# Kernel tuning notes

Hardware: AMD Instinct MI355X
Metric: run time of the kernel (lower is better)

The kernel has to match this reference:

```python
import jax, jax.numpy as jnp
import numpy as np

BATCH = 1024
D_IN = 4096
D_OUT = 4096
B = 128  # block size
K_IN = (D_IN + B - 1) // B    # 32
K_OUT = (D_OUT + B - 1) // B  # 32


def setup_inputs() -> dict:
    key = jax.random.key(0)
    kx, kw, kd = jax.random.split(key, 3)
    x = jax.random.normal(kx, (BATCH, D_IN), dtype=jnp.float32)
    W = jax.random.normal(kw, (K_OUT, K_IN, B), dtype=jnp.float32) * 0.1
    # Bernoulli +/-1 diagonal
    D_bernoulli = jnp.where(jax.random.bernoulli(kd, p=0.5, shape=(D_IN,)), 1.0, -1.0).astype(jnp.float32)
    return {"x": x, "W": W, "D_bernoulli": D_bernoulli}


def reference(x, W, D_bernoulli):
    k_out, k_in, b = W.shape
    d_in = D_IN
    d_out = D_OUT
    if x.ndim == 1:
        x = x[None, :]
    batch = x.shape[0]
    # diagonal sign flip
    x_d = x * D_bernoulli[None, :]
    pad_len = k_in * b - d_in
    if pad_len > 0:
        x_d = jnp.pad(x_d, ((0, 0), (0, pad_len)))
    x_blocks = x_d.reshape(batch, k_in, b)
    # frequency-domain block-circulant matmul
    X_fft = jnp.fft.fft(x_blocks, axis=-1)            # (batch, k_in, b) complex
    W_fft = jnp.fft.fft(W, axis=-1)                    # (k_out, k_in, b) complex
    # Y_fft[n,o,:] = sum_j X_fft[n,j,:] * conj(W_fft[o,j,:])
    Y_fft = jnp.einsum('njb,ojb->nob', X_fft, jnp.conjugate(W_fft))
    Y = jnp.fft.ifft(Y_fft, axis=-1).real              # (batch, k_out, b)
    out_flat = Y.reshape(batch, k_out * b)
    if k_out * b > d_out:
        out_flat = out_flat[:, :d_out]
    return out_flat
```

## Files before the change

kernel.cpp:

```cpp
#include <hip/hip_runtime.h>
#include <hip/hip_bf16.h>

#define TWOPI_OVER_B 0.049087385212340517f

typedef __attribute__((ext_vector_type(8))) short bf16x8;
typedef __attribute__((ext_vector_type(4))) float f32x4;

static __device__ __forceinline__ unsigned short f2bf(float f) {
    __hip_bfloat16 h = __float2bfloat16(f);
    return *reinterpret_cast<unsigned short*>(&h);
}
static __device__ __forceinline__ unsigned long long pack4(float a, float b, float c, float d) {
    return (unsigned long long)f2bf(a) | ((unsigned long long)f2bf(b) << 16)
         | ((unsigned long long)f2bf(c) << 32) | ((unsigned long long)f2bf(d) << 48);
}

__global__ __launch_bounds__(256) void k_prep(const float* __restrict__ W,
                                              unsigned short* __restrict__ fragB,
                                              unsigned short* __restrict__ fragCi,
                                              unsigned short* __restrict__ BmatT) {
    __shared__ char smem[73984];
    int tid = threadIdx.x;

    if (blockIdx.x < 80) {
        int i = blockIdx.x * 256 + tid;
        if (i < 18432) {
            int e = i & 7, l2 = (i >> 3) & 63, kb = (i >> 9) & 3, c = i >> 11;
            int kr = c * 16 + (l2 & 15);
            int t  = kb * 32 + (l2 >> 4) * 8 + e;
            float v = 0.f;
            if (kr < 65)       v =  cosf(TWOPI_OVER_B * (float)((kr * t) & 127));
            else if (kr < 130) v = -sinf(TWOPI_OVER_B * (float)(((kr - 65) * t) & 127));
            fragB[i] = f2bf(v);
        }
        if (i < 20480) {
            int e = i & 7, l2 = (i >> 3) & 63;
            int ckb = i >> 9; int kb = ckb % 5, c = ckb / 5;
            int kr = kb * 32 + (l2 >> 4) * 8 + e;
            int t  = c * 16 + (l2 & 15);
            float v = 0.f;
            if (kr < 65)       v =  cosf(TWOPI_OVER_B * (float)((kr * t) & 127));
            else if (kr < 130) v = -sinf(TWOPI_OVER_B * (float)(((kr - 65) * t) & 127));
            fragCi[i] = f2bf(v);
        }
        return;
    }

    int bw = blockIdx.x - 80;
    unsigned long long* xs8 = (unsigned long long*)smem;
    float* Yl = (float*)smem;
    unsigned short* fB = (unsigned short*)(smem + 37120);

    for (int i = tid; i < 18432; i += 256) {
        int e = i & 7, l2 = (i >> 3) & 63, kb = (i >> 9) & 3, c = i >> 11;
        int kr = c * 16 + (l2 & 15);
        int t  = kb * 32 + (l2 >> 4) * 8 + e;
        float v = 0.f;
        if (kr < 65)       v =  cosf(TWOPI_OVER_B * (float)((kr * t) & 127));
        else if (kr < 130) v = -sinf(TWOPI_OVER_B * (float)(((kr - 65) * t) & 127));
        fB[i] = f2bf(v);
    }
    #pragma unroll
    for (int it = 0; it < 8; ++it) {
        int f  = tid + it * 256;
        float4 wa = ((const float4*)W)[(size_t)bw * 2048 + f];
        int rl = f >> 5;
        int t0 = (f & 31) * 4;
        int byte = (rl * 256 + t0 * 2) ^ ((rl & 7) << 4);
        xs8[byte >> 3] = pack4(wa.x, wa.y, wa.z, wa.w);
    }
    __syncthreads();

    int l = tid & 63, w = tid >> 6;
    int rl_a = w * 16 + (l & 15);
    int coff = (l >> 4) * 16;
    bf16x8 a[4];
    #pragma unroll
    for (int kb = 0; kb < 4; ++kb) {
        int byte = (rl_a * 256 + kb * 64 + coff) ^ ((rl_a & 7) << 4);
        a[kb] = *(const bf16x8*)(smem + byte);
    }
    __syncthreads();

    f32x4 acc[9];
    #pragma unroll
    for (int c = 0; c < 9; ++c) acc[c] = (f32x4)0.f;
    #pragma unroll
    for (int c = 0; c < 9; ++c)
        #pragma unroll
        for (int kb = 0; kb < 4; ++kb)
            acc[c] = __builtin_amdgcn_mfma_f32_16x16x32_bf16(a[kb], ((const bf16x8*)fB)[(c * 4 + kb) * 64 + l], acc[c], 0, 0, 0);

    int rowd = w * 16 + (l >> 4) * 4;
    int cold = l & 15;
    #pragma unroll
    for (int c = 0; c < 9; ++c)
        #pragma unroll
        for (int r = 0; r < 4; ++r)
            Yl[(rowd + r) * 145 + c * 16 + cold] = acc[c][r];
    __syncthreads();

    int o0 = bw * 2;
    for (int c2 = tid; c2 < 4160; c2 += 256) {
        int k = c2 >> 6, sub = c2 & 63;
        int oo = sub >> 5, h = (sub >> 4) & 1, t = sub & 15;
        int j0 = t * 4;
        float sc = (k == 0 || k == 64) ? (1.f / 128.f) : (2.f / 128.f);
        int col; float sgn;
        if (j0 < 32) { col = h ? 65 + k : k;  sgn = h ? -sc : sc; }
        else         { col = h ? k : 65 + k;  sgn = sc; }
        int rlb = oo * 32 + (j0 & 31);
        unsigned long long pk = pack4(sgn * Yl[(rlb + 0) * 145 + col], sgn * Yl[(rlb + 1) * 145 + col],
                                      sgn * Yl[(rlb + 2) * 145 + col], sgn * Yl[(rlb + 3) * 145 + col]);
        int o2 = h * 32 + o0 + oo;
        *(unsigned long long*)(BmatT + ((size_t)k * 64 + o2) * 64 + j0) = pk;
    }
}

#define YS_OFF 33280
__global__ __launch_bounds__(512, 4) void k_fused(const float* __restrict__ x,
                                                  const float* __restrict__ D,
                                                  const bf16x8* __restrict__ fragB,
                                                  const bf16x8* __restrict__ fragCi,
                                                  const unsigned short* __restrict__ BmatT,
                                                  float* __restrict__ out) {
    __shared__ char smem[74240];
    unsigned long long* xs8 = (unsigned long long*)smem;
    int tid = threadIdx.x, l = tid & 63, w = tid >> 6;
    int lr = l & 15, lq = l >> 4;
    int n0 = blockIdx.x * 4;

    #pragma unroll
    for (int it = 0; it < 8; ++it) {
        int f  = tid + it * 512;
        int nn = f >> 10, f4 = f & 1023;
        float4 xa = ((const float4*)(x + (size_t)(n0 + nn) * 4096))[f4];
        float4 da = ((const float4*)D)[f4];
        int rl = nn * 32 + (f4 >> 5);
        int t0 = (f4 & 31) * 4;
        int byte = (rl * 256 + t0 * 2) ^ ((rl & 7) << 4);
        xs8[byte >> 3] = pack4(xa.x * da.x, xa.y * da.y, xa.z * da.z, xa.w * da.w);
    }
    for (int i = tid; i < 3840; i += 512) {
        int rl = i / 30, cp = 130 + i % 30;
        int byte = (rl * 320 + cp * 2) ^ ((rl & 7) << 4);
        *(unsigned short*)(smem + YS_OFF + byte) = 0;
    }
    __syncthreads();

    int rl_a = w * 16 + lr;
    bf16x8 a[4];
    #pragma unroll
    for (int kb = 0; kb < 4; ++kb) {
        int byte = (rl_a * 256 + kb * 64 + lq * 16) ^ ((rl_a & 7) << 4);
        a[kb] = *(const bf16x8*)(smem + byte);
    }
    __syncthreads();

    {
        f32x4 acc[9];
        #pragma unroll
        for (int c = 0; c < 9; ++c) acc[c] = (f32x4)0.f;
        #pragma unroll
        for (int c = 0; c < 9; ++c)
            #pragma unroll
            for (int kb = 0; kb < 4; ++kb)
                acc[c] = __builtin_amdgcn_mfma_f32_16x16x32_bf16(a[kb], fragB[(c * 4 + kb) * 64 + l], acc[c], 0, 0, 0);

        int rowbase = w * 16 + lq * 4;
        #pragma unroll
        for (int c = 0; c < 9; ++c) {
            int col = c * 16 + lr;
            if (col < 130) {
                int k, reim;
                if (col < 65) { k = col;      reim = 0; }
                else          { k = col - 65; reim = 32; }
                #pragma unroll
                for (int rr = 0; rr < 4; ++rr) {
                    int rl2 = rowbase + rr;
                    int nn = rl2 >> 5, j = rl2 & 31;
                    int byte = (k * 512 + nn * 128 + (reim + j) * 2) ^ ((k & 7) << 4);
                    *(unsigned short*)(smem + byte) = f2bf(acc[c][rr]);
                }
            }
        }
    }
    __syncthreads();

    for (int k = w; k < 65; k += 8) {
        int xb = k * 512;
        int swz = (k & 7) << 4;
        bf16x8 a2[2];
        a2[0] = *(const bf16x8*)(smem + ((xb + (lr & 3) * 128 +      lq * 16) ^ swz));
        a2[1] = *(const bf16x8*)(smem + ((xb + (lr & 3) * 128 + 64 + lq * 16) ^ swz));
        const unsigned short* bb = BmatT + (size_t)k * 4096 + lr * 64 + lq * 8;
        f32x4 acc2[4];
        #pragma unroll
        for (int cf = 0; cf < 4; ++cf) acc2[cf] = (f32x4)0.f;
        #pragma unroll
        for (int cf = 0; cf < 4; ++cf) {
            bf16x8 b0 = *(const bf16x8*)(bb + cf * 1024);
            bf16x8 b1 = *(const bf16x8*)(bb + cf * 1024 + 32);
            acc2[cf] = __builtin_amdgcn_mfma_f32_16x16x32_bf16(a2[0], b0, acc2[cf], 0, 0, 0);
            acc2[cf] = __builtin_amdgcn_mfma_f32_16x16x32_bf16(a2[1], b1, acc2[cf], 0, 0, 0);
        }
        if (lq == 0) {
            #pragma unroll
            for (int cf = 0; cf < 4; ++cf) {
                int o2  = cf * 16 + lr;
                int col = (o2 < 32) ? k : 65 + k;
                #pragma unroll
                for (int rr = 0; rr < 4; ++rr) {
                    int row2 = rr * 32 + (o2 & 31);
                    int byte = (row2 * 320 + col * 2) ^ ((row2 & 7) << 4);
                    *(unsigned short*)(smem + YS_OFF + byte) = f2bf(acc2[cf][rr]);
                }
            }
        }
    }
    __syncthreads();

    {
        bf16x8 ac[5];
        #pragma unroll
        for (int kb = 0; kb < 5; ++kb) {
            int byte = (rl_a * 320 + kb * 64 + lq * 16) ^ ((rl_a & 7) << 4);
            ac[kb] = *(const bf16x8*)(smem + YS_OFF + byte);
        }
        f32x4 acc3[8];
        #pragma unroll
        for (int c = 0; c < 8; ++c) acc3[c] = (f32x4)0.f;
        #pragma unroll
        for (int c = 0; c < 8; ++c)
            #pragma unroll
            for (int kb = 0; kb < 5; ++kb)
                acc3[c] = __builtin_amdgcn_mfma_f32_16x16x32_bf16(ac[kb], fragCi[(c * 5 + kb) * 64 + l], acc3[c], 0, 0, 0);

        int rowd = blockIdx.x * 128 + w * 16 + lq * 4;
        #pragma unroll
        for (int c = 0; c < 8; ++c)
            #pragma unroll
            for (int r = 0; r < 4; ++r)
                out[(size_t)(rowd + r) * 128 + c * 16 + lr] = acc3[c][r];
    }
}

extern "C" void kernel_launch(void* const* d_in, const int* in_sizes, int n_in,
                              void* d_out, int out_size, void* d_ws, size_t ws_size,
                              hipStream_t stream) {
    const float* x = (const float*)d_in[0];
    const float* W = (const float*)d_in[1];
    const float* D = (const float*)d_in[2];
    float* out = (float*)d_out;

    unsigned short* BmatT  = (unsigned short*)d_ws;
    unsigned short* fragB  = BmatT + 266240;
    unsigned short* fragCi = fragB + 18432;

    k_prep <<<96, 256, 0, stream>>>(W, fragB, fragCi, BmatT);
    k_fused<<<256, 512, 0, stream>>>(x, D, (const bf16x8*)fragB, (const bf16x8*)fragCi, BmatT, out);
}
```

Before: 50.33 us.

## Halve rows per fused block, prefetch DFT fragments, use sincos table in prep

Fused kernel now processes 2 batch rows per 256-thread block (512 blocks) instead of 4 rows per 512-thread block. Frequency-domain staging moves to a separate LDS region with packed 64-bit writes, which drops one barrier. Global loads of the DFT and weight fragments are software-prefetched one iteration ahead of the MFMAs. k_prep computes a shared cos/sin table once instead of calling transcendentals per element. Smaller blocks should improve occupancy and latency hiding, but each block reloads BmatT for half as many rows, which doubles total weight traffic.

```diff
diff --git a/kernel.cpp b/kernel.cpp
--- a/kernel.cpp
+++ b/kernel.cpp
@@ -20,6 +20,7 @@
                                               unsigned short* __restrict__ fragCi,
                                               unsigned short* __restrict__ BmatT) {
     __shared__ char smem[73984];
+    __shared__ float tbl[256];
     int tid = threadIdx.x;
 
     if (blockIdx.x < 80) {
@@ -51,13 +52,20 @@
     float* Yl = (float*)smem;
     unsigned short* fB = (unsigned short*)(smem + 37120);
 
+    for (int i = tid; i < 128; i += 256) {
+        float s, c;
+        sincosf(TWOPI_OVER_B * (float)i, &s, &c);
+        tbl[i] = c; tbl[128 + i] = s;
+    }
+    __syncthreads();
+
     for (int i = tid; i < 18432; i += 256) {
         int e = i & 7, l2 = (i >> 3) & 63, kb = (i >> 9) & 3, c = i >> 11;
         int kr = c * 16 + (l2 & 15);
         int t  = kb * 32 + (l2 >> 4) * 8 + e;
         float v = 0.f;
-        if (kr < 65)       v =  cosf(TWOPI_OVER_B * (float)((kr * t) & 127));
-        else if (kr < 130) v = -sinf(TWOPI_OVER_B * (float)(((kr - 65) * t) & 127));
+        if (kr < 65)       v =  tbl[(kr * t) & 127];
+        else if (kr < 130) v = -tbl[128 + (((kr - 65) * t) & 127)];
         fB[i] = f2bf(v);
     }
     #pragma unroll
@@ -117,22 +125,23 @@
     }
 }
 
-#define YS_OFF 33280
-__global__ __launch_bounds__(512, 4) void k_fused(const float* __restrict__ x,
-                                                  const float* __restrict__ D,
-                                                  const bf16x8* __restrict__ fragB,
-                                                  const bf16x8* __restrict__ fragCi,
-                                                  const unsigned short* __restrict__ BmatT,
-                                                  float* __restrict__ out) {
-    __shared__ char smem[74240];
+#define XL_OFF 16384
+#define YS_OFF 33024
+__global__ __launch_bounds__(256) void k_fused(const float* __restrict__ x,
+                                               const float* __restrict__ D,
+                                               const bf16x8* __restrict__ fragB,
+                                               const bf16x8* __restrict__ fragCi,
+                                               const unsigned short* __restrict__ BmatT,
+                                               float* __restrict__ out) {
+    __shared__ char smem[53504];
     unsigned long long* xs8 = (unsigned long long*)smem;
     int tid = threadIdx.x, l = tid & 63, w = tid >> 6;
     int lr = l & 15, lq = l >> 4;
-    int n0 = blockIdx.x * 4;
+    int n0 = blockIdx.x * 2;
 
     #pragma unroll
     for (int it = 0; it < 8; ++it) {
-        int f  = tid + it * 512;
+        int f  = tid + it * 256;
         int nn = f >> 10, f4 = f & 1023;
         float4 xa = ((const float4*)(x + (size_t)(n0 + nn) * 4096))[f4];
         float4 da = ((const float4*)D)[f4];
@@ -141,7 +150,7 @@
         int byte = (rl * 256 + t0 * 2) ^ ((rl & 7) << 4);
         xs8[byte >> 3] = pack4(xa.x * da.x, xa.y * da.y, xa.z * da.z, xa.w * da.w);
     }
-    for (int i = tid; i < 3840; i += 512) {
+    for (int i = tid; i < 1920; i += 256) {
         int rl = i / 30, cp = 130 + i % 30;
         int byte = (rl * 320 + cp * 2) ^ ((rl & 7) << 4);
         *(unsigned short*)(smem + YS_OFF + byte) = 0;
@@ -155,66 +164,90 @@
         int byte = (rl_a * 256 + kb * 64 + lq * 16) ^ ((rl_a & 7) << 4);
         a[kb] = *(const bf16x8*)(smem + byte);
     }
-    __syncthreads();
-
     {
+        bf16x8 fb[4], fbn[4];
+        #pragma unroll
+        for (int kb = 0; kb < 4; ++kb) fb[kb] = fragB[kb * 64 + l];
         f32x4 acc[9];
         #pragma unroll
         for (int c = 0; c < 9; ++c) acc[c] = (f32x4)0.f;
         #pragma unroll
-        for (int c = 0; c < 9; ++c)
+        for (int c = 0; c < 9; ++c) {
+            if (c < 8) {
+                #pragma unroll
+                for (int kb = 0; kb < 4; ++kb) fbn[kb] = fragB[((c + 1) * 4 + kb) * 64 + l];
+            }
             #pragma unroll
             for (int kb = 0; kb < 4; ++kb)
-                acc[c] = __builtin_amdgcn_mfma_f32_16x16x32_bf16(a[kb], fragB[(c * 4 + kb) * 64 + l], acc[c], 0, 0, 0);
-
+                acc[c] = __builtin_amdgcn_mfma_f32_16x16x32_bf16(a[kb], fb[kb], acc[c], 0, 0, 0);
+            #pragma unroll
+            for (int kb = 0; kb < 4; ++kb) fb[kb] = fbn[kb];
+        }
         int rowbase = w * 16 + lq * 4;
+        int nn = rowbase >> 5, j0 = rowbase & 31;
         #pragma unroll
         for (int c = 0; c < 9; ++c) {
             int col = c * 16 + lr;
             if (col < 130) {
-                int k, reim;
-                if (col < 65) { k = col;      reim = 0; }
-                else          { k = col - 65; reim = 32; }
+                int k   = (col < 65) ? col : col - 65;
+                int off = (col < 65) ? 0 : 64;
+                unsigned long long pk = pack4(acc[c][0], acc[c][1], acc[c][2], acc[c][3]);
+                int byte = (k * 256 + nn * 128 + off + j0 * 2) ^ ((k & 7) << 4);
+                *(unsigned long long*)(smem + XL_OFF + byte) = pk;
+            }
+        }
+    }
+    __syncthreads();
+
+    {
+        bf16x8 b[4][2], nb[4][2];
+        {
+            const unsigned short* bb = BmatT + (size_t)w * 4096 + lr * 64 + lq * 8;
+            #pragma unroll
+            for (int cf = 0; cf < 4; ++cf) {
+                b[cf][0] = *(const bf16x8*)(bb + cf * 1024);
+                b[cf][1] = *(const bf16x8*)(bb + cf * 1024 + 32);
+            }
+        }
+        for (int k = w; k < 65; k += 4) {
+            int kn = k + 4;
+            if (kn < 65) {
+                const unsigned short* bb = BmatT + (size_t)kn * 4096 + lr * 64 + lq * 8;
                 #pragma unroll
-                for (int rr = 0; rr < 4; ++rr) {
-                    int rl2 = rowbase + rr;
-                    int nn = rl2 >> 5, j = rl2 & 31;
-                    int byte = (k * 512 + nn * 128 + (reim + j) * 2) ^ ((k & 7) << 4);
-                    *(unsigned short*)(smem + byte) = f2bf(acc[c][rr]);
+                for (int cf = 0; cf < 4; ++cf) {
+                    nb[cf][0] = *(const bf16x8*)(bb + cf * 1024);
+                    nb[cf][1] = *(const bf16x8*)(bb + cf * 1024 + 32);
                 }
             }
-        }
-    }
-    __syncthreads();
-
-    for (int k = w; k < 65; k += 8) {
-        int xb = k * 512;
-        int swz = (k & 7) << 4;
-        bf16x8 a2[2];
-        a2[0] = *(const bf16x8*)(smem + ((xb + (lr & 3) * 128 +      lq * 16) ^ swz));
-        a2[1] = *(const bf16x8*)(smem + ((xb + (lr & 3) * 128 + 64 + lq * 16) ^ swz));
-        const unsigned short* bb = BmatT + (size_t)k * 4096 + lr * 64 + lq * 8;
-        f32x4 acc2[4];
-        #pragma unroll
-        for (int cf = 0; cf < 4; ++cf) acc2[cf] = (f32x4)0.f;
-        #pragma unroll
-        for (int cf = 0; cf < 4; ++cf) {
-            bf16x8 b0 = *(const bf16x8*)(bb + cf * 1024);
-            bf16x8 b1 = *(const bf16x8*)(bb + cf * 1024 + 32);
-            acc2[cf] = __builtin_amdgcn_mfma_f32_16x16x32_bf16(a2[0], b0, acc2[cf], 0, 0, 0);
-            acc2[cf] = __builtin_amdgcn_mfma_f32_16x16x32_bf16(a2[1], b1, acc2[cf], 0, 0, 0);
-        }
-        if (lq == 0) {
+            int swz = (k & 7) << 4;
+            int xb = k * 256 + (lr & 1) * 128 + lq * 16;
+            bf16x8 a0 = *(const bf16x8*)(smem + XL_OFF + ((xb)      ^ swz));
+            bf16x8 a1 = *(const bf16x8*)(smem + XL_OFF + ((xb + 64) ^ swz));
+            f32x4 acc2[4];
+            #pragma unroll
+            for (int cf = 0; cf < 4; ++cf) acc2[cf] = (f32x4)0.f;
             #pragma unroll
             for (int cf = 0; cf < 4; ++cf) {
-                int o2  = cf * 16 + lr;
-                int col = (o2 < 32) ? k : 65 + k;
+                acc2[cf] = __builtin_amdgcn_mfma_f32_16x16x32_bf16(a0, b[cf][0], acc2[cf], 0, 0, 0);
+                acc2[cf] = __builtin_amdgcn_mfma_f32_16x16x32_bf16(a1, b[cf][1], acc2[cf], 0, 0, 0);
+            }
+            if (lq == 0) {
                 #pragma unroll
-                for (int rr = 0; rr < 4; ++rr) {
-                    int row2 = rr * 32 + (o2 & 31);
-                    int byte = (row2 * 320 + col * 2) ^ ((row2 & 7) << 4);
-                    *(unsigned short*)(smem + YS_OFF + byte) = f2bf(acc2[cf][rr]);
+                for (int cf = 0; cf < 4; ++cf) {
+                    int o2  = cf * 16 + lr;
+                    int col = (o2 < 32) ? k : 65 + k;
+                    #pragma unroll
+                    for (int rr = 0; rr < 2; ++rr) {
+                        int row2 = rr * 32 + (o2 & 31);
+                        int byte = (row2 * 320 + col * 2) ^ ((row2 & 7) << 4);
+                        *(unsigned short*)(smem + YS_OFF + byte) = f2bf(acc2[cf][rr]);
+                    }
                 }
+            }
+            #pragma unroll
+            for (int cf = 0; cf < 4; ++cf) {
+                b[cf][0] = nb[cf][0];
+                b[cf][1] = nb[cf][1];
             }
         }
     }
@@ -227,16 +260,25 @@
             int byte = (rl_a * 320 + kb * 64 + lq * 16) ^ ((rl_a & 7) << 4);
             ac[kb] = *(const bf16x8*)(smem + YS_OFF + byte);
         }
+        bf16x8 fc[5], fcn[5];
+        #pragma unroll
+        for (int kb = 0; kb < 5; ++kb) fc[kb] = fragCi[kb * 64 + l];
         f32x4 acc3[8];
         #pragma unroll
         for (int c = 0; c < 8; ++c) acc3[c] = (f32x4)0.f;
         #pragma unroll
-        for (int c = 0; c < 8; ++c)
+        for (int c = 0; c < 8; ++c) {
+            if (c < 7) {
+                #pragma unroll
+                for (int kb = 0; kb < 5; ++kb) fcn[kb] = fragCi[((c + 1) * 5 + kb) * 64 + l];
+            }
             #pragma unroll
             for (int kb = 0; kb < 5; ++kb)
-                acc3[c] = __builtin_amdgcn_mfma_f32_16x16x32_bf16(ac[kb], fragCi[(c * 5 + kb) * 64 + l], acc3[c], 0, 0, 0);
-
-        int rowd = blockIdx.x * 128 + w * 16 + lq * 4;
+                acc3[c] = __builtin_amdgcn_mfma_f32_16x16x32_bf16(ac[kb], fc[kb], acc3[c], 0, 0, 0);
+            #pragma unroll
+            for (int kb = 0; kb < 5; ++kb) fc[kb] = fcn[kb];
+        }
+        int rowd = blockIdx.x * 64 + w * 16 + lq * 4;
         #pragma unroll
         for (int c = 0; c < 8; ++c)
             #pragma unroll
@@ -258,5 +300,5 @@
     unsigned short* fragCi = fragB + 18432;
 
     k_prep <<<96, 256, 0, stream>>>(W, fragB, fragCi, BmatT);
-    k_fused<<<256, 512, 0, stream>>>(x, D, (const bf16x8*)fragB, (const bf16x8*)fragCi, BmatT, out);
-}
+    k_fused<<<512, 256, 0, stream>>>(x, D, (const bf16x8*)fragB, (const bf16x8*)fragCi, BmatT, out);
+}
```

New measurement: 60.18 us. 1.2x slower.
